# Performance work log

Hardware: AMD Instinct MI355X
Metric: run time of the kernel (lower is better)

The kernel has to match this reference:

```python
import jax, jax.numpy as jnp
import numpy as np

B, S, D, H = 2, 2048, 1024, 16
DK = D // H

def setup_inputs() -> dict:
    key = jax.random.key(0)
    ks = jax.random.split(key, 5)
    scale = 1.0 / np.sqrt(D)
    return {
        "x": jax.random.normal(ks[0], (B, S, D), dtype=jnp.float32),
        "Wq": jax.random.normal(ks[1], (D, D), dtype=jnp.float32) * scale,
        "bq": jnp.zeros((D,), dtype=jnp.float32),
        "Wk": jax.random.normal(ks[2], (D, D), dtype=jnp.float32) * scale,
        "bk": jnp.zeros((D,), dtype=jnp.float32),
        "Wv": jax.random.normal(ks[3], (D, D), dtype=jnp.float32) * scale,
        "bv": jnp.zeros((D,), dtype=jnp.float32),
        "Wo": jax.random.normal(ks[4], (D, D), dtype=jnp.float32) * scale,
        "bo": jnp.zeros((D,), dtype=jnp.float32),
    }

def _split_heads(t):
    # [B,S,D] -> [B,H,S,DK]
    return t.reshape(B, S, H, DK).transpose(0, 2, 1, 3)

def reference(x, Wq, bq, Wk, bk, Wv, bv, Wo, bo):
    q = _split_heads(x @ Wq.T + bq)
    k = _split_heads(x @ Wk.T + bk)
    v = _split_heads(x @ Wv.T + bv)
    scores = jnp.einsum('bhqd,bhkd->bhqk', q, k) / jnp.sqrt(jnp.float32(DK))
    attn = jax.nn.softmax(scores, axis=-1)  # [B,H,S,S]
    out = jnp.einsum('bhqk,bhkd->bhqd', attn, v)
    out = out.transpose(0, 2, 1, 3).reshape(B, S, D)
    out = out @ Wo.T + bo
    return out, attn
```

## Files before the change

### kernel.cpp

```cpp
#include <hip/hip_runtime.h>

typedef unsigned short u16;
typedef __attribute__((ext_vector_type(8))) short short8;
typedef __attribute__((ext_vector_type(8))) unsigned short us8;
typedef __attribute__((ext_vector_type(4))) unsigned short us4;
typedef __attribute__((ext_vector_type(4))) float f32x4;

namespace {

constexpr int Bn = 2, Sn = 2048, Dn = 1024, Hn = 16, DKn = 64;

__device__ __forceinline__ u16 f2bf(float f) {
  unsigned u = __builtin_bit_cast(unsigned, f);
  u += 0x7fffu + ((u >> 16) & 1u);
  return (u16)(u >> 16);
}
__device__ __forceinline__ float bf2f(u16 h) {
  unsigned u = ((unsigned)h) << 16;
  return __builtin_bit_cast(float, u);
}
__device__ __forceinline__ f32x4 mfma16(short8 a, short8 b, f32x4 c) {
  return __builtin_amdgcn_mfma_f32_16x16x32_bf16(a, b, c, 0, 0, 0);
}
__device__ __forceinline__ void gl_lds16(const void* g, void* l) {
  __builtin_amdgcn_global_load_lds(
      (const __attribute__((address_space(1))) void*)g,
      (__attribute__((address_space(3))) void*)l, 16, 0, 0);
}

__global__ __launch_bounds__(256, 4) void split_f32(
    const float* __restrict__ in, u16* __restrict__ hi, u16* __restrict__ lo, int n) {
  const int i = (blockIdx.x * 256 + threadIdx.x) * 4;
  if (i >= n) return;
  const float4 f = *(const float4*)(in + i);
  const float fs[4] = {f.x, f.y, f.z, f.w};
  us4 hv, lv;
#pragma unroll
  for (int j = 0; j < 4; j++) {
    const u16 h = f2bf(fs[j]);
    hv[j] = h;
    lv[j] = f2bf(fs[j] - bf2f(h));
  }
  *(us4*)(hi + i) = hv;
  *(us4*)(lo + i) = lv;
}

template <bool SPLIT, int OUTMODE>
__global__ __launch_bounds__(256, 2) void proj_gemm(
    const u16* __restrict__ Ah, const u16* __restrict__ Al,
    const u16* __restrict__ Bh, const u16* __restrict__ Bl,
    const float* __restrict__ bias, void* __restrict__ outp) {
  constexpr int K = 1024, BK = 32;
  __shared__ u16 sAh[128 * BK];
  __shared__ u16 sBh[128 * BK];
  __shared__ u16 sAl[SPLIT ? 128 * BK : 16];
  __shared__ u16 sBl[SPLIT ? 128 * BK : 16];
  const int tid = threadIdx.x, l = tid & 63, w = tid >> 6;
  const int m0 = blockIdx.x * 128, n0 = blockIdx.y * 128;
  const int wr = (w >> 1) * 64, wc = (w & 1) * 64;
  const int lr = l & 15, la = l >> 4;
  const int r0 = tid >> 2, q0 = (tid & 3) * 8;
  const int c1 = tid + 256, r1 = c1 >> 2, q1 = (c1 & 3) * 8;
  f32x4 acc[4][4] = {};

  for (int k0 = 0; k0 < K; k0 += BK) {
    __syncthreads();
    gl_lds16(Ah + (size_t)(m0 + r0) * K + k0 + q0, (char*)sAh + tid * 16);
    gl_lds16(Ah + (size_t)(m0 + r1) * K + k0 + q1, (char*)sAh + c1 * 16);
    gl_lds16(Bh + (size_t)(n0 + r0) * K + k0 + q0, (char*)sBh + tid * 16);
    gl_lds16(Bh + (size_t)(n0 + r1) * K + k0 + q1, (char*)sBh + c1 * 16);
    if (SPLIT) {
      gl_lds16(Al + (size_t)(m0 + r0) * K + k0 + q0, (char*)sAl + tid * 16);
      gl_lds16(Al + (size_t)(m0 + r1) * K + k0 + q1, (char*)sAl + c1 * 16);
      gl_lds16(Bl + (size_t)(n0 + r0) * K + k0 + q0, (char*)sBl + tid * 16);
      gl_lds16(Bl + (size_t)(n0 + r1) * K + k0 + q1, (char*)sBl + c1 * 16);
    }
    __syncthreads();

    short8 fah[4], fbh[4];
#pragma unroll
    for (int i = 0; i < 4; i++) {
      fah[i] = *(const short8*)&sAh[(wr + i * 16 + lr) * BK + la * 8];
      fbh[i] = *(const short8*)&sBh[(wc + i * 16 + lr) * BK + la * 8];
    }
    if (SPLIT) {
      short8 fal[4], fbl[4];
#pragma unroll
      for (int i = 0; i < 4; i++) {
        fal[i] = *(const short8*)&sAl[(wr + i * 16 + lr) * BK + la * 8];
        fbl[i] = *(const short8*)&sBl[(wc + i * 16 + lr) * BK + la * 8];
      }
#pragma unroll
      for (int i = 0; i < 4; i++)
#pragma unroll
        for (int j = 0; j < 4; j++) {
          acc[i][j] = mfma16(fah[i], fbh[j], acc[i][j]);
          acc[i][j] = mfma16(fah[i], fbl[j], acc[i][j]);
          acc[i][j] = mfma16(fal[i], fbh[j], acc[i][j]);
        }
    } else {
#pragma unroll
      for (int i = 0; i < 4; i++)
#pragma unroll
        for (int j = 0; j < 4; j++) acc[i][j] = mfma16(fah[i], fbh[j], acc[i][j]);
    }
  }

#pragma unroll
  for (int i = 0; i < 4; i++)
#pragma unroll
    for (int j = 0; j < 4; j++)
#pragma unroll
      for (int r = 0; r < 4; r++) {
        const int m = m0 + wr + i * 16 + la * 4 + r;
        const int n = n0 + wc + j * 16 + lr;
        const float val = acc[i][j][r] + bias[n];
        if (OUTMODE == 0) {
          const int b = m >> 11, s = m & (Sn - 1), h = n >> 6, dk = n & 63;
          ((u16*)outp)[(((size_t)(b * Hn + h)) * Sn + s) * DKn + dk] = f2bf(val);
        } else if (OUTMODE == 1) {
          const int b = m >> 11, s = m & (Sn - 1), h = n >> 6, dk = n & 63;
          ((u16*)outp)[((size_t)(b * Hn + h) * DKn + dk) * Sn + s] = f2bf(val);
        } else {
          ((float*)outp)[(size_t)m * Dn + n] = val;
        }
      }
}

__global__ __launch_bounds__(256, 2) void scores_softmax(
    const u16* __restrict__ q, const u16* __restrict__ kk, float* __restrict__ attn) {
  __shared__ u16 lq[64 * 64];
  __shared__ u16 lk[64 * 64];
  __shared__ float tile[64 * 68];
  __shared__ float rsum[64];
  const int tid = threadIdx.x, l = tid & 63, w = tid >> 6;
  const int bh = blockIdx.y, rt0 = blockIdx.x * 64;
  const int lr = l & 15, la = l >> 4;
  if (tid < 64) rsum[tid] = 0.f;

  const u16* qbase = q + ((size_t)bh * Sn + rt0) * DKn;
  gl_lds16(qbase + tid * 8, (char*)lq + tid * 16);
  gl_lds16(qbase + (tid + 256) * 8, (char*)lq + (tid + 256) * 16);
  __syncthreads();
  short8 qa[4][2];
#pragma unroll
  for (int rt = 0; rt < 4; rt++) {
    qa[rt][0] = *(const short8*)&lq[(rt * 16 + lr) * 64 + la * 8];
    qa[rt][1] = *(const short8*)&lq[(rt * 16 + lr) * 64 + 32 + la * 8];
  }

  const u16* kb0 = kk + (size_t)bh * Sn * DKn;
  float psum[4][4] = {};
  for (int ct = 0; ct < 32; ++ct) {
    __syncthreads();
    const u16* kbase = kb0 + (size_t)ct * 64 * DKn;
    gl_lds16(kbase + tid * 8, (char*)lk + tid * 16);
    gl_lds16(kbase + (tid + 256) * 8, (char*)lk + (tid + 256) * 16);
    __syncthreads();
    const short8 kv0 = *(const short8*)&lk[(w * 16 + lr) * 64 + la * 8];
    const short8 kv1 = *(const short8*)&lk[(w * 16 + lr) * 64 + 32 + la * 8];
#pragma unroll
    for (int rt = 0; rt < 4; rt++) {
      f32x4 sv = {};
      sv = mfma16(qa[rt][0], kv0, sv);
      sv = mfma16(qa[rt][1], kv1, sv);
#pragma unroll
      for (int r = 0; r < 4; r++) psum[rt][r] += __expf(sv[r] * 0.125f);
    }
  }
#pragma unroll
  for (int d = 1; d < 16; d <<= 1)
#pragma unroll
    for (int rt = 0; rt < 4; rt++)
#pragma unroll
      for (int r = 0; r < 4; r++) psum[rt][r] += __shfl_xor(psum[rt][r], d, 64);
  if (lr == 0) {
#pragma unroll
    for (int rt = 0; rt < 4; rt++)
#pragma unroll
      for (int r = 0; r < 4; r++)
        atomicAdd(&rsum[rt * 16 + la * 4 + r], psum[rt][r]);
  }
  __syncthreads();
  float inv[4][4];
#pragma unroll
  for (int rt = 0; rt < 4; rt++)
#pragma unroll
    for (int r = 0; r < 4; r++) inv[rt][r] = 1.0f / rsum[rt * 16 + la * 4 + r];

  float* abase = attn + (size_t)bh * Sn * Sn + (size_t)rt0 * Sn;
  const int srow = tid >> 2, scg = tid & 3;
  for (int ct = 0; ct < 32; ++ct) {
    __syncthreads();
    const u16* kbase = kb0 + (size_t)ct * 64 * DKn;
    gl_lds16(kbase + tid * 8, (char*)lk + tid * 16);
    gl_lds16(kbase + (tid + 256) * 8, (char*)lk + (tid + 256) * 16);
    __syncthreads();
    const short8 kv0 = *(const short8*)&lk[(w * 16 + lr) * 64 + la * 8];
    const short8 kv1 = *(const short8*)&lk[(w * 16 + lr) * 64 + 32 + la * 8];
#pragma unroll
    for (int rt = 0; rt < 4; rt++) {
      f32x4 sv = {};
      sv = mfma16(qa[rt][0], kv0, sv);
      sv = mfma16(qa[rt][1], kv1, sv);
#pragma unroll
      for (int r = 0; r < 4; r++)
        tile[(rt * 16 + la * 4 + r) * 68 + w * 16 + lr] =
            __expf(sv[r] * 0.125f) * inv[rt][r];
    }
    __syncthreads();
    float* dst = abase + (size_t)srow * Sn + ct * 64 + scg * 16;
    const float* srcp = &tile[srow * 68 + scg * 16];
#pragma unroll
    for (int ii = 0; ii < 4; ii++)
      *(float4*)(dst + ii * 4) = *(const float4*)(srcp + ii * 4);
  }
}

__global__ __launch_bounds__(256, 4) void attn_pv(
    const float* __restrict__ attn, const u16* __restrict__ vT,
    u16* __restrict__ chi, u16* __restrict__ clo) {
  __shared__ u16 sA[128 * 64];
  __shared__ u16 sB[64 * 64];
  const int tid = threadIdx.x, l = tid & 63, w = tid >> 6;
  const int bh = blockIdx.y, m0 = blockIdx.x * 128;
  const int b = bh >> 4, h = bh & 15;
  const int lr = l & 15, la = l >> 4;
  const float* Ab = attn + (size_t)bh * Sn * Sn;
  const u16* Bb = vT + (size_t)bh * DKn * Sn;
  const int arow = tid >> 1, ahalf = (tid & 1) * 32;
  const int br0 = tid >> 3, bq0 = (tid & 7) * 8;
  const int c1 = tid + 256, br1 = c1 >> 3, bq1 = (c1 & 7) * 8;
  f32x4 acc[2][4] = {};

  for (int k0 = 0; k0 < Sn; k0 += 64) {
    __syncthreads();
    const float* ap = Ab + (size_t)(m0 + arow) * Sn + k0 + ahalf;
    u16* lp = &sA[arow * 64 + ahalf];
#pragma unroll
    for (int ii = 0; ii < 4; ii++) {
      const float4 f0 = *(const float4*)(ap + ii * 8);
      const float4 f1 = *(const float4*)(ap + ii * 8 + 4);
      us8 pk;
      pk[0] = f2bf(f0.x); pk[1] = f2bf(f0.y); pk[2] = f2bf(f0.z); pk[3] = f2bf(f0.w);
      pk[4] = f2bf(f1.x); pk[5] = f2bf(f1.y); pk[6] = f2bf(f1.z); pk[7] = f2bf(f1.w);
      *(us8*)(lp + ii * 8) = pk;
    }
    gl_lds16(Bb + (size_t)br0 * Sn + k0 + bq0, (char*)sB + tid * 16);
    gl_lds16(Bb + (size_t)br1 * Sn + k0 + bq1, (char*)sB + c1 * 16);
    __syncthreads();

    short8 fa[2][2], fb[4][2];
#pragma unroll
    for (int i = 0; i < 2; i++) {
      fa[i][0] = *(const short8*)&sA[(w * 32 + i * 16 + lr) * 64 + la * 8];
      fa[i][1] = *(const short8*)&sA[(w * 32 + i * 16 + lr) * 64 + 32 + la * 8];
    }
#pragma unroll
    for (int j = 0; j < 4; j++) {
      fb[j][0] = *(const short8*)&sB[(j * 16 + lr) * 64 + la * 8];
      fb[j][1] = *(const short8*)&sB[(j * 16 + lr) * 64 + 32 + la * 8];
    }
#pragma unroll
    for (int i = 0; i < 2; i++)
#pragma unroll
      for (int j = 0; j < 4; j++) {
        acc[i][j] = mfma16(fa[i][0], fb[j][0], acc[i][j]);
        acc[i][j] = mfma16(fa[i][1], fb[j][1], acc[i][j]);
      }
  }

#pragma unroll
  for (int i = 0; i < 2; i++)
#pragma unroll
    for (int j = 0; j < 4; j++)
#pragma unroll
      for (int r = 0; r < 4; r++) {
        const int s = m0 + w * 32 + i * 16 + la * 4 + r;
        const int dd = h * 64 + j * 16 + lr;
        const size_t idx = ((size_t)(b * Sn + s)) * Dn + dd;
        const float v = acc[i][j][r];
        const u16 hv = f2bf(v);
        chi[idx] = hv;
        clo[idx] = f2bf(v - bf2f(hv));
      }
}

}

extern "C" void kernel_launch(void* const* d_in, const int* in_sizes, int n_in,
                              void* d_out, int out_size, void* d_ws, size_t ws_size,
                              hipStream_t stream) {
  (void)in_sizes; (void)n_in; (void)out_size; (void)ws_size;
  const float* x  = (const float*)d_in[0];
  const float* Wq = (const float*)d_in[1];
  const float* bq = (const float*)d_in[2];
  const float* Wk = (const float*)d_in[3];
  const float* bk = (const float*)d_in[4];
  const float* Wv = (const float*)d_in[5];
  const float* bv = (const float*)d_in[6];
  const float* Wo = (const float*)d_in[7];
  const float* bo = (const float*)d_in[8];

  float* out = (float*)d_out;
  float* attn = out + (size_t)Bn * Sn * Dn;

  char* ws = (char*)d_ws;
  auto MB = [](size_t m) { return m << 20; };
  u16* x_hi = (u16*)(ws);
  u16* x_lo = (u16*)(ws + MB(8));
  u16* wq_h = (u16*)(ws + MB(16));
  u16* wq_l = (u16*)(ws + MB(18));
  u16* wk_h = (u16*)(ws + MB(20));
  u16* wk_l = (u16*)(ws + MB(22));
  u16* wv_h = (u16*)(ws + MB(24));
  u16* wv_l = (u16*)(ws + MB(26));
  u16* wo_h = (u16*)(ws + MB(28));
  u16* wo_l = (u16*)(ws + MB(30));
  u16* qb = (u16*)(ws + MB(32));
  u16* kb = (u16*)(ws + MB(40));
  u16* vT = (u16*)(ws + MB(48));
  u16* c_hi = x_hi;
  u16* c_lo = x_lo;

  split_f32<<<4096, 256, 0, stream>>>(x, x_hi, x_lo, Bn * Sn * Dn);
  split_f32<<<1024, 256, 0, stream>>>(Wq, wq_h, wq_l, Dn * Dn);
  split_f32<<<1024, 256, 0, stream>>>(Wk, wk_h, wk_l, Dn * Dn);
  split_f32<<<1024, 256, 0, stream>>>(Wv, wv_h, wv_l, Dn * Dn);
  split_f32<<<1024, 256, 0, stream>>>(Wo, wo_h, wo_l, Dn * Dn);

  proj_gemm<true, 0><<<dim3(32, 8), 256, 0, stream>>>(x_hi, x_lo, wq_h, wq_l, bq, qb);
  proj_gemm<true, 0><<<dim3(32, 8), 256, 0, stream>>>(x_hi, x_lo, wk_h, wk_l, bk, kb);
  proj_gemm<false, 1><<<dim3(32, 8), 256, 0, stream>>>(x_hi, nullptr, wv_h, nullptr, bv, vT);

  scores_softmax<<<dim3(32, 32), 256, 0, stream>>>(qb, kb, attn);
  attn_pv<<<dim3(16, 32), 256, 0, stream>>>(attn, vT, c_hi, c_lo);
  proj_gemm<true, 2><<<dim3(32, 8), 256, 0, stream>>>(c_hi, c_lo, wo_h, wo_l, bo, out);
}
```

Baseline: 1.050 ms.

## Fuse attention-probability times V into the scores/softmax kernel

Computes P·V inside the second pass of the scores/softmax kernel, using the normalized probability tile already in LDS and loading V tiles alongside K tiles. This removes the separate attn_pv kernel, which re-read the full fp32 attention matrix from global memory and converted it to bf16. The cost is extra LDS, extra MFMA and conversion work per tile inside the softmax kernel, and possibly lower occupancy.

```diff
diff --git a/kernel.cpp b/kernel.cpp
--- a/kernel.cpp
+++ b/kernel.cpp
@@ -127,14 +127,18 @@
       }
 }
 
-__global__ __launch_bounds__(256, 2) void scores_softmax(
-    const u16* __restrict__ q, const u16* __restrict__ kk, float* __restrict__ attn) {
+__global__ __launch_bounds__(256, 2) void scores_softmax_pv(
+    const u16* __restrict__ q, const u16* __restrict__ kk,
+    const u16* __restrict__ vT, float* __restrict__ attn,
+    u16* __restrict__ chi, u16* __restrict__ clo) {
   __shared__ u16 lq[64 * 64];
   __shared__ u16 lk[64 * 64];
+  __shared__ u16 lv[64 * 64];
   __shared__ float tile[64 * 68];
   __shared__ float rsum[64];
   const int tid = threadIdx.x, l = tid & 63, w = tid >> 6;
   const int bh = blockIdx.y, rt0 = blockIdx.x * 64;
+  const int b = bh >> 4, h = bh & 15;
   const int lr = l & 15, la = l >> 4;
   if (tid < 64) rsum[tid] = 0.f;
 
@@ -150,6 +154,7 @@
   }
 
   const u16* kb0 = kk + (size_t)bh * Sn * DKn;
+  const u16* vb0 = vT + (size_t)bh * DKn * Sn;
   float psum[4][4] = {};
   for (int ct = 0; ct < 32; ++ct) {
     __syncthreads();
@@ -190,11 +195,16 @@
 
   float* abase = attn + (size_t)bh * Sn * Sn + (size_t)rt0 * Sn;
   const int srow = tid >> 2, scg = tid & 3;
+  const int vr0 = tid >> 3, vq0 = (tid & 7) * 8;
+  const int c1v = tid + 256, vr1 = c1v >> 3, vq1 = (c1v & 7) * 8;
+  f32x4 cacc[4] = {};
   for (int ct = 0; ct < 32; ++ct) {
     __syncthreads();
     const u16* kbase = kb0 + (size_t)ct * 64 * DKn;
     gl_lds16(kbase + tid * 8, (char*)lk + tid * 16);
     gl_lds16(kbase + (tid + 256) * 8, (char*)lk + (tid + 256) * 16);
+    gl_lds16(vb0 + (size_t)vr0 * Sn + ct * 64 + vq0, (char*)lv + tid * 16);
+    gl_lds16(vb0 + (size_t)vr1 * Sn + ct * 64 + vq1, (char*)lv + c1v * 16);
     __syncthreads();
     const short8 kv0 = *(const short8*)&lk[(w * 16 + lr) * 64 + la * 8];
     const short8 kv1 = *(const short8*)&lk[(w * 16 + lr) * 64 + 32 + la * 8];
@@ -214,76 +224,36 @@
 #pragma unroll
     for (int ii = 0; ii < 4; ii++)
       *(float4*)(dst + ii * 4) = *(const float4*)(srcp + ii * 4);
-  }
-}
-
-__global__ __launch_bounds__(256, 4) void attn_pv(
-    const float* __restrict__ attn, const u16* __restrict__ vT,
-    u16* __restrict__ chi, u16* __restrict__ clo) {
-  __shared__ u16 sA[128 * 64];
-  __shared__ u16 sB[64 * 64];
-  const int tid = threadIdx.x, l = tid & 63, w = tid >> 6;
-  const int bh = blockIdx.y, m0 = blockIdx.x * 128;
-  const int b = bh >> 4, h = bh & 15;
-  const int lr = l & 15, la = l >> 4;
-  const float* Ab = attn + (size_t)bh * Sn * Sn;
-  const u16* Bb = vT + (size_t)bh * DKn * Sn;
-  const int arow = tid >> 1, ahalf = (tid & 1) * 32;
-  const int br0 = tid >> 3, bq0 = (tid & 7) * 8;
-  const int c1 = tid + 256, br1 = c1 >> 3, bq1 = (c1 & 7) * 8;
-  f32x4 acc[2][4] = {};
-
-  for (int k0 = 0; k0 < Sn; k0 += 64) {
-    __syncthreads();
-    const float* ap = Ab + (size_t)(m0 + arow) * Sn + k0 + ahalf;
-    u16* lp = &sA[arow * 64 + ahalf];
-#pragma unroll
-    for (int ii = 0; ii < 4; ii++) {
-      const float4 f0 = *(const float4*)(ap + ii * 8);
-      const float4 f1 = *(const float4*)(ap + ii * 8 + 4);
-      us8 pk;
-      pk[0] = f2bf(f0.x); pk[1] = f2bf(f0.y); pk[2] = f2bf(f0.z); pk[3] = f2bf(f0.w);
-      pk[4] = f2bf(f1.x); pk[5] = f2bf(f1.y); pk[6] = f2bf(f1.z); pk[7] = f2bf(f1.w);
-      *(us8*)(lp + ii * 8) = pk;
-    }
-    gl_lds16(Bb + (size_t)br0 * Sn + k0 + bq0, (char*)sB + tid * 16);
-    gl_lds16(Bb + (size_t)br1 * Sn + k0 + bq1, (char*)sB + c1 * 16);
-    __syncthreads();
-
-    short8 fa[2][2], fb[4][2];
-#pragma unroll
-    for (int i = 0; i < 2; i++) {
-      fa[i][0] = *(const short8*)&sA[(w * 32 + i * 16 + lr) * 64 + la * 8];
-      fa[i][1] = *(const short8*)&sA[(w * 32 + i * 16 + lr) * 64 + 32 + la * 8];
-    }
+    const float* prow = &tile[(w * 16 + lr) * 68 + la * 8];
+    us8 a0u, a1u;
+#pragma unroll
+    for (int t = 0; t < 8; t++) {
+      a0u[t] = f2bf(prow[t]);
+      a1u[t] = f2bf(prow[32 + t]);
+    }
+    const short8 pa0 = __builtin_bit_cast(short8, a0u);
+    const short8 pa1 = __builtin_bit_cast(short8, a1u);
 #pragma unroll
     for (int j = 0; j < 4; j++) {
-      fb[j][0] = *(const short8*)&sB[(j * 16 + lr) * 64 + la * 8];
-      fb[j][1] = *(const short8*)&sB[(j * 16 + lr) * 64 + 32 + la * 8];
-    }
-#pragma unroll
-    for (int i = 0; i < 2; i++)
-#pragma unroll
-      for (int j = 0; j < 4; j++) {
-        acc[i][j] = mfma16(fa[i][0], fb[j][0], acc[i][j]);
-        acc[i][j] = mfma16(fa[i][1], fb[j][1], acc[i][j]);
-      }
-  }
-
-#pragma unroll
-  for (int i = 0; i < 2; i++)
-#pragma unroll
-    for (int j = 0; j < 4; j++)
-#pragma unroll
-      for (int r = 0; r < 4; r++) {
-        const int s = m0 + w * 32 + i * 16 + la * 4 + r;
-        const int dd = h * 64 + j * 16 + lr;
-        const size_t idx = ((size_t)(b * Sn + s)) * Dn + dd;
-        const float v = acc[i][j][r];
-        const u16 hv = f2bf(v);
-        chi[idx] = hv;
-        clo[idx] = f2bf(v - bf2f(hv));
-      }
+      const short8 fb0 = *(const short8*)&lv[(j * 16 + lr) * 64 + la * 8];
+      const short8 fb1 = *(const short8*)&lv[(j * 16 + lr) * 64 + 32 + la * 8];
+      cacc[j] = mfma16(pa0, fb0, cacc[j]);
+      cacc[j] = mfma16(pa1, fb1, cacc[j]);
+    }
+  }
+
+#pragma unroll
+  for (int j = 0; j < 4; j++)
+#pragma unroll
+    for (int r = 0; r < 4; r++) {
+      const int s = rt0 + w * 16 + la * 4 + r;
+      const int dd = h * 64 + j * 16 + lr;
+      const size_t idx = ((size_t)(b * Sn + s)) * Dn + dd;
+      const float v = cacc[j][r];
+      const u16 hv = f2bf(v);
+      chi[idx] = hv;
+      clo[idx] = f2bf(v - bf2f(hv));
+    }
 }
 
 }
@@ -333,7 +303,6 @@
   proj_gemm<true, 0><<<dim3(32, 8), 256, 0, stream>>>(x_hi, x_lo, wk_h, wk_l, bk, kb);
   proj_gemm<false, 1><<<dim3(32, 8), 256, 0, stream>>>(x_hi, nullptr, wv_h, nullptr, bv, vT);
 
-  scores_softmax<<<dim3(32, 32), 256, 0, stream>>>(qb, kb, attn);
-  attn_pv<<<dim3(16, 32), 256, 0, stream>>>(attn, vT, c_hi, c_lo);
+  scores_softmax_pv<<<dim3(32, 32), 256, 0, stream>>>(qb, kb, vT, attn, c_hi, c_lo);
   proj_gemm<true, 2><<<dim3(32, 8), 256, 0, stream>>>(c_hi, c_lo, wo_h, wo_l, bo, out);
 }
```

Result: faster. 905.4 us (-13.8%).
